# Kernel optimization log

Measured on AMD Instinct MI355X. Metric: run time of the kernel, lower is better.

The kernel has to match this reference:

```python
import jax, jax.numpy as jnp
import numpy as np

L, B, D, H = 2048, 2, 1024, 16


def setup_inputs() -> dict:
    key = jax.random.key(0)
    ks = jax.random.split(key, 4)
    x = jax.random.normal(ks[0], (L, B, D), dtype=jnp.float32)
    W_in = jax.random.normal(ks[1], (3 * D, D), dtype=jnp.float32) * (1.0 / np.sqrt(D))
    b_in = jnp.zeros((3 * D,), dtype=jnp.float32)
    W_out = jax.random.normal(ks[2], (D, D), dtype=jnp.float32) * (1.0 / np.sqrt(D))
    b_out = jnp.zeros((D,), dtype=jnp.float32)
    mask = jnp.zeros((1, L, L), dtype=jnp.float32)
    return {"q": x, "k": x, "v": x, "mask": mask,
            "W_in": W_in, "b_in": b_in, "W_out": W_out, "b_out": b_out,
            "num_heads": H}


def reference(q, k, v, mask, W_in, b_in, W_out, b_out, num_heads):
    l, b, d = q.shape
    hd = d // num_heads
    # fused QKV projection (q == k == v in this module)
    qkv = q @ W_in.T + b_in                      # (l, b, 3d)
    qh, kh, vh = jnp.split(qkv, 3, axis=-1)      # each (l, b, d)

    def to_heads(t):
        # (l, b, d) -> (b*h, l, hd)
        return t.reshape(l, b * num_heads, hd).transpose(1, 0, 2)

    qh, kh, vh = to_heads(qh), to_heads(kh), to_heads(vh)
    qh = qh / jnp.sqrt(jnp.asarray(hd, dtype=qh.dtype))
    scores = jnp.einsum('nld,nmd->nlm', qh, kh) + mask   # (b*h, l, l)
    attn = jax.nn.softmax(scores, axis=-1)
    z = jnp.einsum('nlm,nmd->nld', attn, vh)             # (b*h, l, hd)
    z = z.transpose(1, 0, 2).reshape(l * b, d)
    z = z @ W_out.T + b_out
    return z.reshape(l, b, d)
```

## Files before the change

### kernel.cpp

```cpp
#include <hip/hip_runtime.h>


typedef short  s8v  __attribute__((ext_vector_type(8)));
typedef short  s4vv __attribute__((ext_vector_type(4)));
typedef float  f4v  __attribute__((ext_vector_type(4)));
typedef float  f4l  __attribute__((ext_vector_type(4)));
typedef float  f16v __attribute__((ext_vector_type(16)));
typedef int    i4v  __attribute__((ext_vector_type(4)));
typedef int    i2v  __attribute__((ext_vector_type(2)));

__device__ __forceinline__ short f2bf(float f) {
  union { float f; unsigned u; } x; x.f = f;
  unsigned r = (x.u + 0x7fffu + ((x.u >> 16) & 1u)) >> 16;
  return (short)r;
}

__device__ __forceinline__ int cvtpk(float lo, float hi) {
  int r;
  asm("v_cvt_pk_bf16_f32 %0, %1, %2" : "=v"(r) : "v"(lo), "v"(hi));
  return r;
}

#define GLDS16(gp, lp) __builtin_amdgcn_global_load_lds( \
    (const __attribute__((address_space(1))) void*)(gp),  \
    (__attribute__((address_space(3))) void*)(lp), 16, 0, 0)

#define LOG2E 1.4426950408889634f

__global__ __launch_bounds__(256) void cast3(const float* __restrict__ x,
                                             const float* __restrict__ wi,
                                             const float* __restrict__ wo,
                                             short* __restrict__ xb,
                                             short* __restrict__ wib,
                                             short* __restrict__ wob) {
  int i = blockIdx.x * 256 + threadIdx.x;
  const float* src; short* dst; int off;
  if (i < 1048576)            { src = x;  dst = xb;  off = i; }
  else if (i < 1048576 + 786432) { src = wi; dst = wib; off = i - 1048576; }
  else                        { src = wo; dst = wob; off = i - 1835008; }
  f4l v = ((const f4l*)src)[off];
  s4vv o;
  o[0] = f2bf(v[0]); o[1] = f2bf(v[1]); o[2] = f2bf(v[2]); o[3] = f2bf(v[3]);
  ((s4vv*)dst)[off] = o;
}

__global__ __launch_bounds__(256) void mask_scan(const float* __restrict__ mask,
                                                 unsigned* __restrict__ flags) {
  const int l = blockIdx.x;
  const int qt = l >> 7;
  const int t = threadIdx.x;
  const float* row = mask + ((size_t)l << 11) + (t << 3);
  f4l a = *(const f4l*)row;
  f4l b = *(const f4l*)(row + 4);
  bool nz = (a[0] != 0.f) | (a[1] != 0.f) | (a[2] != 0.f) | (a[3] != 0.f) |
            (b[0] != 0.f) | (b[1] != 0.f) | (b[2] != 0.f) | (b[3] != 0.f);
  unsigned long long bal = __ballot(nz);
  const int w = t >> 6, lane = t & 63;
  if (lane == 0 && bal) {
    unsigned bits = 0;
#pragma unroll
    for (int g = 0; g < 8; ++g)
      if ((bal >> (g << 3)) & 0xFFull) bits |= 1u << ((w << 3) + g);
    atomicOr(&flags[qt], bits);
  }
}

__global__ __launch_bounds__(256) void gemm_qkv(const short* __restrict__ A,
                                                const short* __restrict__ B,
                                                const float* __restrict__ bin,
                                                short* __restrict__ Qh,
                                                short* __restrict__ Kh,
                                                short* __restrict__ Vh) {
  __shared__ __align__(16) short As[128 * 64];
  __shared__ __align__(16) short Bs[128 * 64];
  const int tid = threadIdx.x;
  const int w = tid >> 6, lane = tid & 63;
  const int g = lane >> 4, c15 = lane & 15;
  const int wr = w >> 1, wc = w & 1;
  const int rowbase = blockIdx.y << 7;
  const int colbase = blockIdx.x << 7;
  const int rl = lane >> 3, sp = lane & 7;
  const int swz = (sp ^ rl) << 3;

  f4v acc[4][4] = {};

  for (int kt = 0; kt < 16; ++kt) {
#pragma unroll
    for (int c2 = 0; c2 < 4; ++c2) {
      const int chunk = (w << 2) + c2;
      const int row = (chunk << 3) + rl;
      GLDS16(A + ((size_t)(rowbase + row) << 10) + (kt << 6) + swz, &As[chunk << 9]);
      GLDS16(B + ((size_t)(colbase + row) << 10) + (kt << 6) + swz, &Bs[chunk << 9]);
    }
    __syncthreads();
#pragma unroll
    for (int kk = 0; kk < 2; ++kk) {
      s8v af[4], bf[4];
#pragma unroll
      for (int m = 0; m < 4; ++m) {
        const int row = (wr << 6) + (m << 4) + c15;
        af[m] = *(const s8v*)((const char*)As + row * 128 + ((((kk << 2) | g) ^ (row & 7)) << 4));
        const int col = (wc << 6) + (m << 4) + c15;
        bf[m] = *(const s8v*)((const char*)Bs + col * 128 + ((((kk << 2) | g) ^ (col & 7)) << 4));
      }
#pragma unroll
      for (int m = 0; m < 4; ++m)
#pragma unroll
        for (int nn = 0; nn < 4; ++nn)
          acc[m][nn] = __builtin_amdgcn_mfma_f32_16x16x32_bf16(af[m], bf[nn], acc[m][nn], 0, 0, 0);
    }
    __syncthreads();
  }

  const int r0 = rowbase + (wr << 6) + (g << 2);
  const int c0 = colbase + (wc << 6) + c15;
#pragma unroll
  for (int nn = 0; nn < 4; ++nn) {
    const int col = c0 + (nn << 4);
    const int which = col >> 10;
    const int dd = col & 1023;
    const int hh = dd >> 6, ee = dd & 63;
    const float bias = bin[col];
    const float mul = (which == 0) ? 0.125f * LOG2E : 1.0f;
    short* dst = (which == 0) ? Qh : ((which == 1) ? Kh : Vh);
#pragma unroll
    for (int m = 0; m < 4; ++m) {
#pragma unroll
      for (int j = 0; j < 4; ++j) {
        const int row = r0 + (m << 4) + j;
        const int li = row >> 1, bb = row & 1;
        const int nh = (bb << 4) + hh;
        dst[(((size_t)nh * 2048 + li) << 6) + ee] = f2bf((acc[m][nn][j] + bias) * mul);
      }
    }
  }
}

__global__ __launch_bounds__(256) void vtrans(const short* __restrict__ Vh,
                                              short* __restrict__ VT) {
  __shared__ short t[64][264];
  const int n = blockIdx.x, lt = blockIdx.y;
  const int tid = threadIdx.x;
  const short* src = Vh + (((size_t)n * 2048 + (lt << 8) + tid) << 6);
#pragma unroll
  for (int c = 0; c < 8; ++c) {
    s8v v = *(const s8v*)(src + (c << 3));
#pragma unroll
    for (int j = 0; j < 8; ++j) t[(c << 3) + j][tid] = v[j];
  }
  __syncthreads();
  const int d = tid >> 2, l0 = (tid & 3) << 6;
  short* dst = VT + ((((size_t)n << 6) + d) << 11) + (lt << 8) + l0;
#pragma unroll
  for (int c = 0; c < 8; ++c)
    *(s8v*)(dst + (c << 3)) = *(const s8v*)(&t[d][l0 + (c << 3)]);
}

__global__ __launch_bounds__(256) void gemm_out(const short* __restrict__ A,
                                                const short* __restrict__ B,
                                                const float* __restrict__ bout,
                                                float* __restrict__ out) {
  __shared__ __align__(16) short As[128 * 64];
  __shared__ __align__(16) short Bs[128 * 64];
  const int tid = threadIdx.x;
  const int w = tid >> 6, lane = tid & 63;
  const int g = lane >> 4, c15 = lane & 15;
  const int wr = w >> 1, wc = w & 1;
  const int rowbase = blockIdx.y << 7;
  const int colbase = blockIdx.x << 7;
  const int rl = lane >> 3, sp = lane & 7;
  const int swz = (sp ^ rl) << 3;

  f4v acc[4][4] = {};

  for (int kt = 0; kt < 16; ++kt) {
#pragma unroll
    for (int c2 = 0; c2 < 4; ++c2) {
      const int chunk = (w << 2) + c2;
      const int row = (chunk << 3) + rl;
      GLDS16(A + ((size_t)(rowbase + row) << 10) + (kt << 6) + swz, &As[chunk << 9]);
      GLDS16(B + ((size_t)(colbase + row) << 10) + (kt << 6) + swz, &Bs[chunk << 9]);
    }
    __syncthreads();
#pragma unroll
    for (int kk = 0; kk < 2; ++kk) {
      s8v af[4], bf[4];
#pragma unroll
      for (int m = 0; m < 4; ++m) {
        const int row = (wr << 6) + (m << 4) + c15;
        af[m] = *(const s8v*)((const char*)As + row * 128 + ((((kk << 2) | g) ^ (row & 7)) << 4));
        const int col = (wc << 6) + (m << 4) + c15;
        bf[m] = *(const s8v*)((const char*)Bs + col * 128 + ((((kk << 2) | g) ^ (col & 7)) << 4));
      }
#pragma unroll
      for (int m = 0; m < 4; ++m)
#pragma unroll
        for (int nn = 0; nn < 4; ++nn)
          acc[m][nn] = __builtin_amdgcn_mfma_f32_16x16x32_bf16(af[m], bf[nn], acc[m][nn], 0, 0, 0);
    }
    __syncthreads();
  }

  const int r0 = rowbase + (wr << 6) + (g << 2);
  const int c0 = colbase + (wc << 6) + c15;
#pragma unroll
  for (int nn = 0; nn < 4; ++nn) {
    const int col = c0 + (nn << 4);
    const float bias = bout[col];
#pragma unroll
    for (int m = 0; m < 4; ++m) {
#pragma unroll
      for (int j = 0; j < 4; ++j) {
        const int row = r0 + (m << 4) + j;
        out[((size_t)row << 10) + col] = acc[m][nn][j] + bias;
      }
    }
  }
}

__global__ __launch_bounds__(256, 2) void attn(const short* __restrict__ Qh,
                                               const short* __restrict__ Kh,
                                               const short* __restrict__ VTg,
                                               const float* __restrict__ mask,
                                               const unsigned* __restrict__ mflags,
                                               short* __restrict__ Z) {
  __shared__ __align__(16) short Ks[3][64 * 64];
  __shared__ __align__(16) short Vs[3][64 * 64];
  const int tid = threadIdx.x;
  const int w = tid >> 6, lane = tid & 63;
  const int q5 = lane & 31, hi = lane >> 5;
  const int orig = blockIdx.x;
  const int wg = ((orig & 7) << 6) + (orig >> 3);
  const int n = wg >> 4, qt = wg & 15;
  const int srow8 = lane >> 3, sp = lane & 7;
  const int ssw = (sp ^ srow8) << 3;

  const int qg = (qt << 7) + (w << 5) + q5;

  const short* Qp = Qh + (((size_t)n * 2048 + qg) << 6);
  s8v bq[4];
#pragma unroll
  for (int ks = 0; ks < 4; ++ks)
    bq[ks] = *(const s8v*)(Qp + (ks << 4) + (hi << 3));

  const short* Kbase = Kh + ((size_t)n << 17);
  const short* Vbase = VTg + ((size_t)n << 17);
  const float* mrow = mask + ((size_t)qg << 11) + (hi << 2);
  const unsigned mbits = mflags[qt];
  const int kslot = q5 & 7;

  f16v oA0, oA1, zz;
#pragma unroll
  for (int e = 0; e < 16; ++e) { oA0[e] = 0.0f; oA1[e] = 0.0f; zz[e] = 0.0f; }
  float ls0 = 0.0f, ls1 = 0.0f;

#define VMW(N) asm volatile("s_waitcnt vmcnt(" #N ")" ::: "memory")
#define BAR()  do { __builtin_amdgcn_s_barrier(); asm volatile("" ::: "memory"); } while (0)

#define STAGEK(bi, t) do { const int cw = w << 1;                               \
    GLDS16(Kbase + ((size_t)(((t) << 6) + (cw << 3) + srow8) << 6) + ssw,       \
           &Ks[bi][cw << 9]);                                                   \
    GLDS16(Kbase + ((size_t)(((t) << 6) + ((cw + 1) << 3) + srow8) << 6) + ssw, \
           &Ks[bi][(cw + 1) << 9]); } while (0)
#define STAGEV(bi, t) do { const int cw = w << 1;                               \
    GLDS16(Vbase + ((size_t)((cw << 3) + srow8) << 11) + ((t) << 6) + ssw,      \
           &Vs[bi][cw << 9]);                                                   \
    GLDS16(Vbase + ((size_t)(((cw + 1) << 3) + srow8) << 11) + ((t) << 6) + ssw,\
           &Vs[bi][(cw + 1) << 9]); } while (0)

#define QKM(S0_, S1_, bi) do {                                                  \
    const char* Kc = (const char*)&Ks[bi][0];                                   \
    __builtin_amdgcn_s_setprio(1);                                              \
    _Pragma("unroll")                                                           \
    for (int ks = 0; ks < 4; ++ks) {                                            \
      const int so = ((2 * ks + hi) ^ kslot) << 4;                              \
      s8v ak0 = *(const s8v*)(Kc + q5 * 128 + so);                              \
      s8v ak1 = *(const s8v*)(Kc + (q5 + 32) * 128 + so);                       \
      if (ks == 0) {                                                            \
        S0_ = __builtin_amdgcn_mfma_f32_32x32x16_bf16(ak0, bq[0], zz, 0, 0, 0); \
        S1_ = __builtin_amdgcn_mfma_f32_32x32x16_bf16(ak1, bq[0], zz, 0, 0, 0); \
      } else {                                                                  \
        S0_ = __builtin_amdgcn_mfma_f32_32x32x16_bf16(ak0, bq[ks], S0_, 0,0,0); \
        S1_ = __builtin_amdgcn_mfma_f32_32x32x16_bf16(ak1, bq[ks], S1_, 0,0,0); \
      } }                                                                       \
    __builtin_amdgcn_s_setprio(0); } while (0)

#define SMPV(S0_, S1_, t, bi) do {                                              \
    if ((mbits >> (t)) & 1u) {                                                  \
      const float* mp = mrow + ((t) << 6);                                      \
      _Pragma("unroll")                                                         \
      for (int c = 0; c < 4; ++c) {                                             \
        f4l mv0 = *(const f4l*)(mp + (c << 3));                                 \
        f4l mv1 = *(const f4l*)(mp + 32 + (c << 3));                            \
        _Pragma("unroll")                                                       \
        for (int j = 0; j < 4; ++j) {                                           \
          S0_[(c << 2) + j] += mv0[j] * LOG2E;                                  \
          S1_[(c << 2) + j] += mv1[j] * LOG2E;                                  \
        } } }                                                                   \
    _Pragma("unroll")                                                           \
    for (int r = 0; r < 16; ++r) {                                              \
      float a = __builtin_amdgcn_exp2f(S0_[r]); S0_[r] = a; ls0 += a;           \
      float b = __builtin_amdgcn_exp2f(S1_[r]); S1_[r] = b; ls1 += b;           \
    }                                                                           \
    const char* Vc = (const char*)&Vs[bi][0];                                   \
    __builtin_amdgcn_s_setprio(1);                                              \
    _Pragma("unroll")                                                           \
    for (int ks = 0; ks < 4; ++ks) {                                            \
      const f16v& sv = (ks < 2) ? S0_ : S1_;                                    \
      const int ro = (ks & 1) << 3;                                             \
      int P0 = cvtpk(sv[ro + 0], sv[ro + 1]);                                   \
      int P1 = cvtpk(sv[ro + 2], sv[ro + 3]);                                   \
      int P2 = cvtpk(sv[ro + 4], sv[ro + 5]);                                   \
      int P3 = cvtpk(sv[ro + 6], sv[ro + 7]);                                   \
      int x0 = __shfl_xor(P2, 32);                                              \
      int x1 = __shfl_xor(P3, 32);                                              \
      int x2 = __shfl_xor(P0, 32);                                              \
      int x3 = __shfl_xor(P1, 32);                                              \
      union { i4v i; s8v s; } pu;                                               \
      pu.i[0] = hi ? x0 : P0;                                                   \
      pu.i[1] = hi ? x1 : P1;                                                   \
      pu.i[2] = hi ? P2 : x2;                                                   \
      pu.i[3] = hi ? P3 : x3;                                                   \
      const int so = ((2 * ks + hi) ^ kslot) << 4;                              \
      s8v av0 = *(const s8v*)(Vc + q5 * 128 + so);                              \
      s8v av1 = *(const s8v*)(Vc + (q5 + 32) * 128 + so);                       \
      oA0 = __builtin_amdgcn_mfma_f32_32x32x16_bf16(av0, pu.s, oA0, 0, 0, 0);   \
      oA1 = __builtin_amdgcn_mfma_f32_32x32x16_bf16(av1, pu.s, oA1, 0, 0, 0);   \
    }                                                                           \
    __builtin_amdgcn_s_setprio(0); } while (0)

  f16v sA0, sA1, sB0, sB1;

  asm volatile("s_waitcnt vmcnt(0)" ::: "memory");
  STAGEK(0, 0); STAGEV(0, 0); STAGEK(1, 1); STAGEV(1, 1); STAGEK(2, 2);
  VMW(8);
  BAR();
  QKM(sA0, sA1, 0);
  VMW(4);
  BAR();

  int bc = 0;
  for (int p = 0; p < 28; p += 2) {
    const int b1 = (bc == 2) ? 0 : bc + 1;
    const int b2 = (b1 == 2) ? 0 : b1 + 1;
    STAGEK(bc, p + 3);
    STAGEV(b2, p + 2);
    QKM(sB0, sB1, b1);
    SMPV(sA0, sA1, p, bc);
    VMW(4); BAR();
    STAGEK(b1, p + 4);
    STAGEV(bc, p + 3);
    QKM(sA0, sA1, b2);
    SMPV(sB0, sB1, p + 1, b1);
    VMW(4); BAR();
    bc = b2;
  }
  STAGEK(1, 31);
  STAGEV(0, 30);
  QKM(sB0, sB1, 2);
  SMPV(sA0, sA1, 28, 1);
  VMW(4); BAR();
  STAGEV(1, 31);
  QKM(sA0, sA1, 0);
  SMPV(sB0, sB1, 29, 2);
  VMW(2); BAR();
  QKM(sB0, sB1, 1);
  SMPV(sA0, sA1, 30, 0);
  VMW(0); BAR();
  SMPV(sB0, sB1, 31, 1);

#undef STAGEK
#undef STAGEV
#undef QKM
#undef SMPV
#undef VMW
#undef BAR

  float lrun = ls0 + ls1;
  lrun += __shfl_xor(lrun, 32);
  const float invl = 1.0f / lrun;
  short* zp = Z + ((((size_t)qg << 1) + (n >> 4)) << 10) + ((n & 15) << 6);
#pragma unroll
  for (int c = 0; c < 4; ++c) {
    const int d0 = (c << 3) + (hi << 2);
    i2v w0, w1;
    w0[0] = cvtpk(oA0[(c << 2) + 0] * invl, oA0[(c << 2) + 1] * invl);
    w0[1] = cvtpk(oA0[(c << 2) + 2] * invl, oA0[(c << 2) + 3] * invl);
    *(i2v*)(zp + d0) = w0;
    w1[0] = cvtpk(oA1[(c << 2) + 0] * invl, oA1[(c << 2) + 1] * invl);
    w1[1] = cvtpk(oA1[(c << 2) + 2] * invl, oA1[(c << 2) + 3] * invl);
    *(i2v*)(zp + 32 + d0) = w1;
  }
}

extern "C" void kernel_launch(void* const* d_in, const int* in_sizes, int n_in,
                              void* d_out, int out_size, void* d_ws, size_t ws_size,
                              hipStream_t stream) {
  const float* xq   = (const float*)d_in[0];
  const float* mask = (const float*)d_in[3];
  const float* Win  = (const float*)d_in[4];
  const float* bin  = (const float*)d_in[5];
  const float* Wout = (const float*)d_in[6];
  const float* bout = (const float*)d_in[7];
  float* out = (float*)d_out;

  char* ws = (char*)d_ws;
  short* xb  = (short*)(ws);
  short* wib = (short*)(ws + (8ull  << 20));
  short* wob = (short*)(ws + (14ull << 20));
  short* Qh  = (short*)(ws + (16ull << 20));
  short* Kh  = (short*)(ws + (24ull << 20));
  short* Vh  = (short*)(ws + (32ull << 20));
  short* VTg = (short*)(ws + (40ull << 20));
  short* Zb  = (short*)(ws + (48ull << 20));
  unsigned* mflags = (unsigned*)(ws + (56ull << 20));

  hipMemsetAsync(mflags, 0, 16 * sizeof(unsigned), stream);
  cast3<<<8192, 256, 0, stream>>>(xq, Win, Wout, xb, wib, wob);
  mask_scan<<<2048, 256, 0, stream>>>(mask, mflags);
  gemm_qkv<<<dim3(24, 32), 256, 0, stream>>>(xb, wib, bin, Qh, Kh, Vh);
  vtrans<<<dim3(32, 8), 256, 0, stream>>>(Vh, VTg);
  attn<<<512, 256, 0, stream>>>(Qh, Kh, VTg, mask, mflags, Zb);
  gemm_out<<<dim3(8, 32), 256, 0, stream>>>(Zb, wob, bout, out);
}
```

Measured before the change: 140.0 us.

## Split attention KV tile across two wave groups and merge partial outputs via LDS

```diff
diff --git a/kernel.cpp b/kernel.cpp
--- a/kernel.cpp
+++ b/kernel.cpp
@@ -218,7 +218,7 @@
   }
 }
 
-__global__ __launch_bounds__(256, 2) void attn(const short* __restrict__ Qh,
+__global__ __launch_bounds__(512, 4) void attn(const short* __restrict__ Qh,
                                                const short* __restrict__ Kh,
                                                const short* __restrict__ VTg,
                                                const float* __restrict__ mask,
@@ -229,15 +229,17 @@
   const int tid = threadIdx.x;
   const int w = tid >> 6, lane = tid & 63;
   const int q5 = lane & 31, hi = lane >> 5;
+  const int qgl = w & 3, kh = w >> 2;
+  const int khb = kh << 5;
   const int orig = blockIdx.x;
   const int wg = ((orig & 7) << 6) + (orig >> 3);
   const int n = wg >> 4, qt = wg & 15;
   const int srow8 = lane >> 3, sp = lane & 7;
   const int ssw = (sp ^ srow8) << 3;
 
-  const int qg = (qt << 7) + (w << 5) + q5;
-
-  const short* Qp = Qh + (((size_t)n * 2048 + qg) << 6);
+  const int qglob = (qt << 7) + (qgl << 5) + q5;
+
+  const short* Qp = Qh + (((size_t)n * 2048 + qglob) << 6);
   s8v bq[4];
 #pragma unroll
   for (int ks = 0; ks < 4; ++ks)
@@ -245,73 +247,57 @@
 
   const short* Kbase = Kh + ((size_t)n << 17);
   const short* Vbase = VTg + ((size_t)n << 17);
-  const float* mrow = mask + ((size_t)qg << 11) + (hi << 2);
+  const float* mrow = mask + ((size_t)qglob << 11) + (hi << 2);
   const unsigned mbits = mflags[qt];
   const int kslot = q5 & 7;
 
   f16v oA0, oA1, zz;
 #pragma unroll
   for (int e = 0; e < 16; ++e) { oA0[e] = 0.0f; oA1[e] = 0.0f; zz[e] = 0.0f; }
-  float ls0 = 0.0f, ls1 = 0.0f;
+  float ls = 0.0f;
 
 #define VMW(N) asm volatile("s_waitcnt vmcnt(" #N ")" ::: "memory")
 #define BAR()  do { __builtin_amdgcn_s_barrier(); asm volatile("" ::: "memory"); } while (0)
 
-#define STAGEK(bi, t) do { const int cw = w << 1;                               \
-    GLDS16(Kbase + ((size_t)(((t) << 6) + (cw << 3) + srow8) << 6) + ssw,       \
-           &Ks[bi][cw << 9]);                                                   \
-    GLDS16(Kbase + ((size_t)(((t) << 6) + ((cw + 1) << 3) + srow8) << 6) + ssw, \
-           &Ks[bi][(cw + 1) << 9]); } while (0)
-#define STAGEV(bi, t) do { const int cw = w << 1;                               \
-    GLDS16(Vbase + ((size_t)((cw << 3) + srow8) << 11) + ((t) << 6) + ssw,      \
-           &Vs[bi][cw << 9]);                                                   \
-    GLDS16(Vbase + ((size_t)(((cw + 1) << 3) + srow8) << 11) + ((t) << 6) + ssw,\
-           &Vs[bi][(cw + 1) << 9]); } while (0)
-
-#define QKM(S0_, S1_, bi) do {                                                  \
+#define STAGEK(bi, t) GLDS16(Kbase + ((size_t)(((t) << 6) + (w << 3) + srow8) << 6) + ssw, \
+                             &Ks[bi][w << 9])
+#define STAGEV(bi, t) GLDS16(Vbase + ((size_t)((w << 3) + srow8) << 11) + ((t) << 6) + ssw, \
+                             &Vs[bi][w << 9])
+
+#define QKM(S_, bi) do {                                                        \
     const char* Kc = (const char*)&Ks[bi][0];                                   \
     __builtin_amdgcn_s_setprio(1);                                              \
     _Pragma("unroll")                                                           \
     for (int ks = 0; ks < 4; ++ks) {                                            \
       const int so = ((2 * ks + hi) ^ kslot) << 4;                              \
-      s8v ak0 = *(const s8v*)(Kc + q5 * 128 + so);                              \
-      s8v ak1 = *(const s8v*)(Kc + (q5 + 32) * 128 + so);                       \
-      if (ks == 0) {                                                            \
-        S0_ = __builtin_amdgcn_mfma_f32_32x32x16_bf16(ak0, bq[0], zz, 0, 0, 0); \
-        S1_ = __builtin_amdgcn_mfma_f32_32x32x16_bf16(ak1, bq[0], zz, 0, 0, 0); \
-      } else {                                                                  \
-        S0_ = __builtin_amdgcn_mfma_f32_32x32x16_bf16(ak0, bq[ks], S0_, 0,0,0); \
-        S1_ = __builtin_amdgcn_mfma_f32_32x32x16_bf16(ak1, bq[ks], S1_, 0,0,0); \
-      } }                                                                       \
+      s8v ak = *(const s8v*)(Kc + (khb + q5) * 128 + so);                       \
+      if (ks == 0) S_ = __builtin_amdgcn_mfma_f32_32x32x16_bf16(ak, bq[0], zz, 0, 0, 0); \
+      else         S_ = __builtin_amdgcn_mfma_f32_32x32x16_bf16(ak, bq[ks], S_, 0, 0, 0); \
+    }                                                                           \
     __builtin_amdgcn_s_setprio(0); } while (0)
 
-#define SMPV(S0_, S1_, t, bi) do {                                              \
+#define SMPV(S_, t, bi) do {                                                    \
     if ((mbits >> (t)) & 1u) {                                                  \
-      const float* mp = mrow + ((t) << 6);                                      \
+      const float* mp = mrow + ((t) << 6) + khb;                                \
       _Pragma("unroll")                                                         \
       for (int c = 0; c < 4; ++c) {                                             \
-        f4l mv0 = *(const f4l*)(mp + (c << 3));                                 \
-        f4l mv1 = *(const f4l*)(mp + 32 + (c << 3));                            \
+        f4l mv = *(const f4l*)(mp + (c << 3));                                  \
         _Pragma("unroll")                                                       \
-        for (int j = 0; j < 4; ++j) {                                           \
-          S0_[(c << 2) + j] += mv0[j] * LOG2E;                                  \
-          S1_[(c << 2) + j] += mv1[j] * LOG2E;                                  \
-        } } }                                                                   \
+        for (int j = 0; j < 4; ++j) S_[(c << 2) + j] += mv[j] * LOG2E;          \
+      } }                                                                       \
     _Pragma("unroll")                                                           \
     for (int r = 0; r < 16; ++r) {                                              \
-      float a = __builtin_amdgcn_exp2f(S0_[r]); S0_[r] = a; ls0 += a;           \
-      float b = __builtin_amdgcn_exp2f(S1_[r]); S1_[r] = b; ls1 += b;           \
+      float a = __builtin_amdgcn_exp2f(S_[r]); S_[r] = a; ls += a;              \
     }                                                                           \
     const char* Vc = (const char*)&Vs[bi][0];                                   \
     __builtin_amdgcn_s_setprio(1);                                              \
     _Pragma("unroll")                                                           \
-    for (int ks = 0; ks < 4; ++ks) {                                            \
-      const f16v& sv = (ks < 2) ? S0_ : S1_;                                    \
-      const int ro = (ks & 1) << 3;                                             \
-      int P0 = cvtpk(sv[ro + 0], sv[ro + 1]);                                   \
-      int P1 = cvtpk(sv[ro + 2], sv[ro + 3]);                                   \
-      int P2 = cvtpk(sv[ro + 4], sv[ro + 5]);                                   \
-      int P3 = cvtpk(sv[ro + 6], sv[ro + 7]);                                   \
+    for (int ks2 = 0; ks2 < 2; ++ks2) {                                         \
+      const int ro = ks2 << 3;                                                  \
+      int P0 = cvtpk(S_[ro + 0], S_[ro + 1]);                                   \
+      int P1 = cvtpk(S_[ro + 2], S_[ro + 3]);                                   \
+      int P2 = cvtpk(S_[ro + 4], S_[ro + 5]);                                   \
+      int P3 = cvtpk(S_[ro + 6], S_[ro + 7]);                                   \
       int x0 = __shfl_xor(P2, 32);                                              \
       int x1 = __shfl_xor(P3, 32);                                              \
       int x2 = __shfl_xor(P0, 32);                                              \
@@ -321,7 +307,7 @@
       pu.i[1] = hi ? x1 : P1;                                                   \
       pu.i[2] = hi ? P2 : x2;                                                   \
       pu.i[3] = hi ? P3 : x3;                                                   \
-      const int so = ((2 * ks + hi) ^ kslot) << 4;                              \
+      const int so = (((kh << 2) + (ks2 << 1) + hi) ^ kslot) << 4;              \
       s8v av0 = *(const s8v*)(Vc + q5 * 128 + so);                              \
       s8v av1 = *(const s8v*)(Vc + (q5 + 32) * 128 + so);                       \
       oA0 = __builtin_amdgcn_mfma_f32_32x32x16_bf16(av0, pu.s, oA0, 0, 0, 0);   \
@@ -329,14 +315,14 @@
     }                                                                           \
     __builtin_amdgcn_s_setprio(0); } while (0)
 
-  f16v sA0, sA1, sB0, sB1;
+  f16v sA, sB;
 
   asm volatile("s_waitcnt vmcnt(0)" ::: "memory");
   STAGEK(0, 0); STAGEV(0, 0); STAGEK(1, 1); STAGEV(1, 1); STAGEK(2, 2);
-  VMW(8);
+  VMW(4);
   BAR();
-  QKM(sA0, sA1, 0);
-  VMW(4);
+  QKM(sA, 0);
+  VMW(2);
   BAR();
 
   int bc = 0;
@@ -345,29 +331,29 @@
     const int b2 = (b1 == 2) ? 0 : b1 + 1;
     STAGEK(bc, p + 3);
     STAGEV(b2, p + 2);
-    QKM(sB0, sB1, b1);
-    SMPV(sA0, sA1, p, bc);
-    VMW(4); BAR();
+    QKM(sB, b1);
+    SMPV(sA, p, bc);
+    VMW(2); BAR();
     STAGEK(b1, p + 4);
     STAGEV(bc, p + 3);
-    QKM(sA0, sA1, b2);
-    SMPV(sB0, sB1, p + 1, b1);
-    VMW(4); BAR();
+    QKM(sA, b2);
+    SMPV(sB, p + 1, b1);
+    VMW(2); BAR();
     bc = b2;
   }
   STAGEK(1, 31);
   STAGEV(0, 30);
-  QKM(sB0, sB1, 2);
-  SMPV(sA0, sA1, 28, 1);
-  VMW(4); BAR();
+  QKM(sB, 2);
+  SMPV(sA, 28, 1);
+  VMW(2); BAR();
   STAGEV(1, 31);
-  QKM(sA0, sA1, 0);
-  SMPV(sB0, sB1, 29, 2);
-  VMW(2); BAR();
-  QKM(sB0, sB1, 1);
-  SMPV(sA0, sA1, 30, 0);
+  QKM(sA, 0);
+  SMPV(sB, 29, 2);
+  VMW(1); BAR();
+  QKM(sB, 1);
+  SMPV(sA, 30, 0);
   VMW(0); BAR();
-  SMPV(sB0, sB1, 31, 1);
+  SMPV(sB, 31, 1);
 
 #undef STAGEK
 #undef STAGEV
@@ -376,20 +362,34 @@
 #undef VMW
 #undef BAR
 
-  float lrun = ls0 + ls1;
-  lrun += __shfl_xor(lrun, 32);
-  const float invl = 1.0f / lrun;
-  short* zp = Z + ((((size_t)qg << 1) + (n >> 4)) << 10) + ((n & 15) << 6);
-#pragma unroll
-  for (int c = 0; c < 4; ++c) {
-    const int d0 = (c << 3) + (hi << 2);
-    i2v w0, w1;
-    w0[0] = cvtpk(oA0[(c << 2) + 0] * invl, oA0[(c << 2) + 1] * invl);
-    w0[1] = cvtpk(oA0[(c << 2) + 2] * invl, oA0[(c << 2) + 3] * invl);
-    *(i2v*)(zp + d0) = w0;
-    w1[0] = cvtpk(oA1[(c << 2) + 0] * invl, oA1[(c << 2) + 1] * invl);
-    w1[1] = cvtpk(oA1[(c << 2) + 2] * invl, oA1[(c << 2) + 3] * invl);
-    *(i2v*)(zp + 32 + d0) = w1;
+  float ts = ls + __shfl_xor(ls, 32);
+  __syncthreads();
+  float* fb = (float*)&Ks[0][0];
+  if (kh == 1) {
+    float* p = fb + ((qgl << 6) + lane) * 34;
+#pragma unroll
+    for (int e = 0; e < 16; ++e) { p[e] = oA0[e]; p[16 + e] = oA1[e]; }
+    p[32] = ts;
+  }
+  __syncthreads();
+  if (kh == 0) {
+    const float* p = fb + ((qgl << 6) + lane) * 34;
+#pragma unroll
+    for (int e = 0; e < 16; ++e) { oA0[e] += p[e]; oA1[e] += p[16 + e]; }
+    ts += p[32];
+    const float invl = 1.0f / ts;
+    short* zp = Z + ((((size_t)qglob << 1) + (n >> 4)) << 10) + ((n & 15) << 6);
+#pragma unroll
+    for (int c = 0; c < 4; ++c) {
+      const int d0 = (c << 3) + (hi << 2);
+      i2v w0, w1;
+      w0[0] = cvtpk(oA0[(c << 2) + 0] * invl, oA0[(c << 2) + 1] * invl);
+      w0[1] = cvtpk(oA0[(c << 2) + 2] * invl, oA0[(c << 2) + 3] * invl);
+      *(i2v*)(zp + d0) = w0;
+      w1[0] = cvtpk(oA1[(c << 2) + 0] * invl, oA1[(c << 2) + 1] * invl);
+      w1[1] = cvtpk(oA1[(c << 2) + 2] * invl, oA1[(c << 2) + 3] * invl);
+      *(i2v*)(zp + 32 + d0) = w1;
+    }
   }
 }
 
@@ -420,6 +420,6 @@
   mask_scan<<<2048, 256, 0, stream>>>(mask, mflags);
   gemm_qkv<<<dim3(24, 32), 256, 0, stream>>>(xb, wib, bin, Qh, Kh, Vh);
   vtrans<<<dim3(32, 8), 256, 0, stream>>>(Vh, VTg);
-  attn<<<512, 256, 0, stream>>>(Qh, Kh, VTg, mask, mflags, Zb);
+  attn<<<512, 512, 0, stream>>>(Qh, Kh, VTg, mask, mflags, Zb);
   gemm_out<<<dim3(8, 32), 256, 0, stream>>>(Zb, wob, bout, out);
 }
```

Result: slower. 178.5 us (+27.6%).

## Fuse cast and mask-scan kernels; write V transposed directly from QKV GEMM

Applied to the files above, without the earlier changes.

```diff
diff --git a/kernel.cpp b/kernel.cpp
--- a/kernel.cpp
+++ b/kernel.cpp
@@ -27,41 +27,43 @@
 
 #define LOG2E 1.4426950408889634f
 
-__global__ __launch_bounds__(256) void cast3(const float* __restrict__ x,
-                                             const float* __restrict__ wi,
-                                             const float* __restrict__ wo,
-                                             short* __restrict__ xb,
-                                             short* __restrict__ wib,
-                                             short* __restrict__ wob) {
-  int i = blockIdx.x * 256 + threadIdx.x;
-  const float* src; short* dst; int off;
-  if (i < 1048576)            { src = x;  dst = xb;  off = i; }
-  else if (i < 1048576 + 786432) { src = wi; dst = wib; off = i - 1048576; }
-  else                        { src = wo; dst = wob; off = i - 1835008; }
-  f4l v = ((const f4l*)src)[off];
-  s4vv o;
-  o[0] = f2bf(v[0]); o[1] = f2bf(v[1]); o[2] = f2bf(v[2]); o[3] = f2bf(v[3]);
-  ((s4vv*)dst)[off] = o;
-}
-
-__global__ __launch_bounds__(256) void mask_scan(const float* __restrict__ mask,
-                                                 unsigned* __restrict__ flags) {
-  const int l = blockIdx.x;
-  const int qt = l >> 7;
-  const int t = threadIdx.x;
-  const float* row = mask + ((size_t)l << 11) + (t << 3);
-  f4l a = *(const f4l*)row;
-  f4l b = *(const f4l*)(row + 4);
-  bool nz = (a[0] != 0.f) | (a[1] != 0.f) | (a[2] != 0.f) | (a[3] != 0.f) |
-            (b[0] != 0.f) | (b[1] != 0.f) | (b[2] != 0.f) | (b[3] != 0.f);
-  unsigned long long bal = __ballot(nz);
-  const int w = t >> 6, lane = t & 63;
-  if (lane == 0 && bal) {
-    unsigned bits = 0;
-#pragma unroll
-    for (int g = 0; g < 8; ++g)
-      if ((bal >> (g << 3)) & 0xFFull) bits |= 1u << ((w << 3) + g);
-    atomicOr(&flags[qt], bits);
+__global__ __launch_bounds__(256) void prep(const float* __restrict__ x,
+                                            const float* __restrict__ wi,
+                                            const float* __restrict__ wo,
+                                            const float* __restrict__ mask,
+                                            short* __restrict__ xb,
+                                            short* __restrict__ wib,
+                                            short* __restrict__ wob,
+                                            unsigned* __restrict__ flags) {
+  const int b = blockIdx.x;
+  if (b < 8192) {
+    int i = b * 256 + threadIdx.x;
+    const float* src; short* dst; int off;
+    if (i < 1048576)               { src = x;  dst = xb;  off = i; }
+    else if (i < 1048576 + 786432) { src = wi; dst = wib; off = i - 1048576; }
+    else                           { src = wo; dst = wob; off = i - 1835008; }
+    f4l v = ((const f4l*)src)[off];
+    s4vv o;
+    o[0] = f2bf(v[0]); o[1] = f2bf(v[1]); o[2] = f2bf(v[2]); o[3] = f2bf(v[3]);
+    ((s4vv*)dst)[off] = o;
+  } else {
+    const int l = b - 8192;
+    const int qt = l >> 7;
+    const int t = threadIdx.x;
+    const float* row = mask + ((size_t)l << 11) + (t << 3);
+    f4l a = *(const f4l*)row;
+    f4l bb = *(const f4l*)(row + 4);
+    bool nz = (a[0] != 0.f) | (a[1] != 0.f) | (a[2] != 0.f) | (a[3] != 0.f) |
+              (bb[0] != 0.f) | (bb[1] != 0.f) | (bb[2] != 0.f) | (bb[3] != 0.f);
+    unsigned long long bal = __ballot(nz);
+    const int w = t >> 6, lane = t & 63;
+    if (lane == 0 && bal) {
+      unsigned bits = 0;
+#pragma unroll
+      for (int g = 0; g < 8; ++g)
+        if ((bal >> (g << 3)) & 0xFFull) bits |= 1u << ((w << 3) + g);
+      atomicOr(&flags[qt], bits);
+    }
   }
 }
 
@@ -70,7 +72,7 @@
                                                 const float* __restrict__ bin,
                                                 short* __restrict__ Qh,
                                                 short* __restrict__ Kh,
-                                                short* __restrict__ Vh) {
+                                                short* __restrict__ VT) {
   __shared__ __align__(16) short As[128 * 64];
   __shared__ __align__(16) short Bs[128 * 64];
   const int tid = threadIdx.x;
@@ -114,46 +116,37 @@
 
   const int r0 = rowbase + (wr << 6) + (g << 2);
   const int c0 = colbase + (wc << 6) + c15;
+  const int which = colbase >> 10;
 #pragma unroll
   for (int nn = 0; nn < 4; ++nn) {
     const int col = c0 + (nn << 4);
-    const int which = col >> 10;
     const int dd = col & 1023;
     const int hh = dd >> 6, ee = dd & 63;
     const float bias = bin[col];
-    const float mul = (which == 0) ? 0.125f * LOG2E : 1.0f;
-    short* dst = (which == 0) ? Qh : ((which == 1) ? Kh : Vh);
-#pragma unroll
-    for (int m = 0; m < 4; ++m) {
-#pragma unroll
-      for (int j = 0; j < 4; ++j) {
-        const int row = r0 + (m << 4) + j;
-        const int li = row >> 1, bb = row & 1;
-        const int nh = (bb << 4) + hh;
-        dst[(((size_t)nh * 2048 + li) << 6) + ee] = f2bf((acc[m][nn][j] + bias) * mul);
+    if (which == 2) {
+      unsigned* v0p = (unsigned*)(VT + ((((size_t)hh << 6) + ee) << 11));
+      unsigned* v1p = (unsigned*)(VT + (((((size_t)hh + 16) << 6) + ee) << 11));
+#pragma unroll
+      for (int m = 0; m < 4; ++m) {
+        const int li0 = (r0 >> 1) + (m << 3);
+        v0p[li0 >> 1] = (unsigned)cvtpk(acc[m][nn][0] + bias, acc[m][nn][2] + bias);
+        v1p[li0 >> 1] = (unsigned)cvtpk(acc[m][nn][1] + bias, acc[m][nn][3] + bias);
       }
-    }
-  }
-}
-
-__global__ __launch_bounds__(256) void vtrans(const short* __restrict__ Vh,
-                                              short* __restrict__ VT) {
-  __shared__ short t[64][264];
-  const int n = blockIdx.x, lt = blockIdx.y;
-  const int tid = threadIdx.x;
-  const short* src = Vh + (((size_t)n * 2048 + (lt << 8) + tid) << 6);
-#pragma unroll
-  for (int c = 0; c < 8; ++c) {
-    s8v v = *(const s8v*)(src + (c << 3));
-#pragma unroll
-    for (int j = 0; j < 8; ++j) t[(c << 3) + j][tid] = v[j];
-  }
-  __syncthreads();
-  const int d = tid >> 2, l0 = (tid & 3) << 6;
-  short* dst = VT + ((((size_t)n << 6) + d) << 11) + (lt << 8) + l0;
-#pragma unroll
-  for (int c = 0; c < 8; ++c)
-    *(s8v*)(dst + (c << 3)) = *(const s8v*)(&t[d][l0 + (c << 3)]);
+    } else {
+      const float mul = (which == 0) ? 0.125f * LOG2E : 1.0f;
+      short* dst = (which == 0) ? Qh : Kh;
+#pragma unroll
+      for (int m = 0; m < 4; ++m) {
+#pragma unroll
+        for (int j = 0; j < 4; ++j) {
+          const int row = r0 + (m << 4) + j;
+          const int li = row >> 1, bb = row & 1;
+          const int nh = (bb << 4) + hh;
+          dst[(((size_t)nh * 2048 + li) << 6) + ee] = f2bf((acc[m][nn][j] + bias) * mul);
+        }
+      }
+    }
+  }
 }
 
 __global__ __launch_bounds__(256) void gemm_out(const short* __restrict__ A,
@@ -410,16 +403,13 @@
   short* wob = (short*)(ws + (14ull << 20));
   short* Qh  = (short*)(ws + (16ull << 20));
   short* Kh  = (short*)(ws + (24ull << 20));
-  short* Vh  = (short*)(ws + (32ull << 20));
-  short* VTg = (short*)(ws + (40ull << 20));
-  short* Zb  = (short*)(ws + (48ull << 20));
-  unsigned* mflags = (unsigned*)(ws + (56ull << 20));
+  short* VTg = (short*)(ws + (32ull << 20));
+  short* Zb  = (short*)(ws + (40ull << 20));
+  unsigned* mflags = (unsigned*)(ws + (48ull << 20));
 
   hipMemsetAsync(mflags, 0, 16 * sizeof(unsigned), stream);
-  cast3<<<8192, 256, 0, stream>>>(xq, Win, Wout, xb, wib, wob);
-  mask_scan<<<2048, 256, 0, stream>>>(mask, mflags);
-  gemm_qkv<<<dim3(24, 32), 256, 0, stream>>>(xb, wib, bin, Qh, Kh, Vh);
-  vtrans<<<dim3(32, 8), 256, 0, stream>>>(Vh, VTg);
+  prep<<<8192 + 2048, 256, 0, stream>>>(xq, Win, Wout, mask, xb, wib, wob, mflags);
+  gemm_qkv<<<dim3(24, 32), 256, 0, stream>>>(xb, wib, bin, Qh, Kh, VTg);
   attn<<<512, 256, 0, stream>>>(Qh, Kh, VTg, mask, mflags, Zb);
   gemm_out<<<dim3(8, 32), 256, 0, stream>>>(Zb, wob, bout, out);
 }
```

Result: no change. 138.6 us (-1.0%).
